# Kernel tuning notes

Hardware: AMD Instinct MI355X
Metric: run time of the kernel (lower is better)

Reference implementation:

```python
import jax, jax.numpy as jnp
import numpy as np

NUM_NODES = 100000
NUM_EDGES = 50000
NUM_CONN = 800000
IN_DIM = 256
HIDDEN = 128
EDGE_ATTR_DIM = 17
LN_EPS = 1e-5


def setup_inputs() -> dict:
    key = jax.random.key(0)
    k1, k2, k3, kw1, kb1, kg, kbeta, kw2, kb2 = jax.random.split(key, 9)
    node_features = jax.random.normal(k1, (NUM_NODES, IN_DIM), dtype=jnp.float32)
    nodes = jax.random.randint(k2, (NUM_CONN,), 0, NUM_NODES, dtype=jnp.int64)
    edges = jax.random.randint(k3, (NUM_CONN,), 0, NUM_EDGES, dtype=jnp.int64)
    hyperedge_index = jnp.stack([nodes, edges], axis=0)
    # MLP params (Linear(in,hid) -> LayerNorm -> ReLU -> Dropout(eval:identity) -> Linear(hid,out))
    W1 = jax.random.normal(kw1, (IN_DIM, HIDDEN), dtype=jnp.float32) * (1.0 / np.sqrt(IN_DIM))
    b1 = jax.random.normal(kb1, (HIDDEN,), dtype=jnp.float32) * 0.01
    ln_g = jnp.ones((HIDDEN,), dtype=jnp.float32)
    ln_b = jnp.zeros((HIDDEN,), dtype=jnp.float32)
    W2 = jax.random.normal(kw2, (HIDDEN, EDGE_ATTR_DIM), dtype=jnp.float32) * (1.0 / np.sqrt(HIDDEN))
    b2 = jax.random.normal(kb2, (EDGE_ATTR_DIM,), dtype=jnp.float32) * 0.01
    return {"node_features": node_features, "hyperedge_index": hyperedge_index,
            "W1": W1, "b1": b1, "ln_g": ln_g, "ln_b": ln_b, "W2": W2, "b2": b2}


def reference(node_features, hyperedge_index, W1, b1, ln_g, ln_b, W2, b2):
    nodes = hyperedge_index[0]
    edges = hyperedge_index[1]
    # indices are in-range by construction (torch valid_mask is all-True here)
    gathered = node_features[nodes]                         # [num_conn, in_dim]
    summed = jax.ops.segment_sum(gathered, edges, num_segments=NUM_EDGES)
    counts = jax.ops.segment_sum(jnp.ones(edges.shape, node_features.dtype), edges,
                                 num_segments=NUM_EDGES)
    edge_features = summed / jnp.clip(counts, 1.0)[:, None]  # mean aggregation
    # decoder MLP (dropout inactive in eval)
    h = edge_features @ W1 + b1
    mu = jnp.mean(h, axis=-1, keepdims=True)
    var = jnp.mean(jnp.square(h - mu), axis=-1, keepdims=True)
    h = (h - mu) * jax.lax.rsqrt(var + LN_EPS) * ln_g + ln_b
    h = jax.nn.relu(h)
    return h @ W2 + b2                                      # [num_edges, edge_attr_dim]
```

## Files before the change

kernel.cpp:

```cpp
#include <hip/hip_runtime.h>
#include <hip/hip_bf16.h>
#include <stdint.h>

#define NUM_NODES 100000
#define NUM_EDGES 50000
#define NUM_CONN  800000
#define IN_DIM    256
#define HIDDEN    128
#define EDGE_DIM  17
#define PAD       64

typedef __bf16 bf16x8 __attribute__((ext_vector_type(8)));
typedef float  f32x4  __attribute__((ext_vector_type(4)));


__global__ void prep_kernel(const float* __restrict__ W1, const float* __restrict__ W2,
                            __bf16* __restrict__ w1f, __bf16* __restrict__ w2f,
                            int* __restrict__ counts) {
    int i = blockIdx.x * 256 + threadIdx.x;
    if (i < NUM_EDGES) counts[i] = 0;
    if (i < 4096) {
        int lane = i & 63, t = (i >> 6) & 7, kc2 = i >> 9;
        int m = lane & 15, q = lane >> 4;
        int n = t * 16 + m;
        int kbase = kc2 * 32 + q * 8;
        __bf16* dst = w1f + (size_t)i * 8;
        #pragma unroll
        for (int ki = 0; ki < 8; ++ki)
            dst[ki] = (__bf16)W1[(size_t)(kbase + ki) * HIDDEN + n];
    } else if (i < 4608) {
        int f = i - 4096;
        int lane = f & 63, t = (f >> 6) & 1, ks = f >> 7;
        int m = lane & 15, q = lane >> 4;
        int n = t * 16 + m;
        int kbase = ks * 32 + q * 8;
        __bf16* dst = w2f + (size_t)f * 8;
        #pragma unroll
        for (int ki = 0; ki < 8; ++ki)
            dst[ki] = (n < EDGE_DIM) ? (__bf16)W2[(size_t)(kbase + ki) * EDGE_DIM + n]
                                     : (__bf16)0.0f;
    }
}

#define FRONT_BLOCKS 1173
__global__ __launch_bounds__(256) void front_kernel(const int* __restrict__ idx,
        int stride, int* __restrict__ counts, int* __restrict__ slots,
        const float* __restrict__ nf, const __bf16* __restrict__ w1f,
        __bf16* __restrict__ pbf) {
    __shared__ __align__(16) __bf16 lds_w[32768];
    const int d3 = blockIdx.x / 3, r3 = blockIdx.x % 3;
    if (r3 == 1) {
        long c0 = ((long)d3 * 256 + threadIdx.x) * 8;
        if (c0 < NUM_CONN) {
            int nd[8], ed[8];
            if (stride == 2) {
                #pragma unroll
                for (int k = 0; k < 4; ++k) {
                    int4 vn = ((const int4*)idx)[c0 / 2 + k];
                    int4 ve = ((const int4*)(idx + 2 * NUM_CONN))[c0 / 2 + k];
                    nd[2 * k] = vn.x; nd[2 * k + 1] = vn.z;
                    ed[2 * k] = ve.x; ed[2 * k + 1] = ve.z;
                }
            } else {
                #pragma unroll
                for (int k = 0; k < 8; ++k) {
                    nd[k] = idx[c0 + k];
                    ed[k] = idx[NUM_CONN + c0 + k];
                }
            }
            int pos[8];
            #pragma unroll
            for (int k = 0; k < 8; ++k) pos[k] = atomicAdd(&counts[ed[k]], 1);
            #pragma unroll
            for (int k = 0; k < 8; ++k)
                if (pos[k] < PAD) slots[(size_t)ed[k] * PAD + pos[k]] = nd[k];
        }
        return;
    }
    const int p = 2 * d3 + (r3 == 2 ? 1 : 0);
    {
        const uint4* src = (const uint4*)w1f;
        uint4* dst = (uint4*)lds_w;
        #pragma unroll
        for (int i = threadIdx.x; i < 4096; i += 256) dst[i] = src[i];
    }
    __syncthreads();

    const int wave = threadIdx.x >> 6;
    const int lane = threadIdx.x & 63;
    const int m = lane & 15, q = lane >> 4;
    const int rowbase = p * 128 + wave * 32;
    const bf16x8* frag = (const bf16x8*)lds_w;

    const float* ap[2];
    #pragma unroll
    for (int mt = 0; mt < 2; ++mt) {
        int r = rowbase + mt * 16 + m;
        if (r >= NUM_NODES) r = NUM_NODES - 1;
        ap[mt] = nf + (size_t)r * IN_DIM + q * 8;
    }

    f32x4 acc[2][8];
    #pragma unroll
    for (int mt = 0; mt < 2; ++mt)
        #pragma unroll
        for (int t = 0; t < 8; ++t) acc[mt][t] = (f32x4){0.f, 0.f, 0.f, 0.f};

    float4 a4[16];
    #pragma unroll
    for (int kc2 = 0; kc2 < 8; ++kc2) {
        a4[2 * kc2]     = *(const float4*)(ap[0] + kc2 * 32);
        a4[2 * kc2 + 1] = *(const float4*)(ap[0] + kc2 * 32 + 4);
    }

    #pragma unroll
    for (int mt = 0; mt < 2; ++mt) {
        bf16x8 afr[8];
        #pragma unroll
        for (int kc2 = 0; kc2 < 8; ++kc2) {
            float4 f0 = a4[2 * kc2], f1 = a4[2 * kc2 + 1];
            afr[kc2][0] = (__bf16)f0.x; afr[kc2][1] = (__bf16)f0.y;
            afr[kc2][2] = (__bf16)f0.z; afr[kc2][3] = (__bf16)f0.w;
            afr[kc2][4] = (__bf16)f1.x; afr[kc2][5] = (__bf16)f1.y;
            afr[kc2][6] = (__bf16)f1.z; afr[kc2][7] = (__bf16)f1.w;
        }
        if (mt == 0) {
            #pragma unroll
            for (int kc2 = 0; kc2 < 8; ++kc2) {
                a4[2 * kc2]     = *(const float4*)(ap[1] + kc2 * 32);
                a4[2 * kc2 + 1] = *(const float4*)(ap[1] + kc2 * 32 + 4);
            }
        }
        #pragma unroll
        for (int kc2 = 0; kc2 < 8; ++kc2) {
            #pragma unroll
            for (int t = 0; t < 8; ++t)
                acc[mt][t] = __builtin_amdgcn_mfma_f32_16x16x32_bf16(
                    afr[kc2], frag[(kc2 * 8 + t) * 64 + lane], acc[mt][t], 0, 0, 0);
        }
    }

    #pragma unroll
    for (int mt = 0; mt < 2; ++mt) {
        int ob = rowbase + mt * 16 + q * 4;
        #pragma unroll
        for (int t = 0; t < 8; ++t)
            #pragma unroll
            for (int r = 0; r < 4; ++r) {
                int orow = ob + r;
                if (orow < NUM_NODES)
                    pbf[(size_t)orow * HIDDEN + t * 16 + m] = (__bf16)acc[mt][t][r];
            }
    }
}

__global__ __launch_bounds__(256) void edge_kernel(const uint4* __restrict__ p4,
        const int* __restrict__ counts, const int* __restrict__ slots,
        const float* __restrict__ b1, const float* __restrict__ ln_g,
        const float* __restrict__ ln_b, const __bf16* __restrict__ w2f,
        const float* __restrict__ b2, float* __restrict__ out) {
    __shared__ __align__(16) uint4 lds_r[256];
    const int wave = threadIdx.x >> 6;
    const int lane = threadIdx.x & 63;
    const int g = lane & 15, ge = lane >> 4;
    const int el = wave * 4 + ge;
    const int e = blockIdx.x * 16 + el;

    const int c = counts[e];
    const int cc = c < PAD ? c : PAD;
    const float inv = 1.0f / (float)(c > 0 ? c : 1);

    float acc[8];
    #pragma unroll
    for (int d = 0; d < 8; ++d) acc[d] = 0.f;

    for (int c0 = 0; c0 < cc; c0 += 16) {
        int slv = slots[(size_t)e * PAD + c0 + g];
        int lim = cc - c0; if (lim > 16) lim = 16;
        if (lim == 16) {
            #pragma unroll
            for (int k0 = 0; k0 < 16; k0 += 4) {
                uint4 u[4];
                #pragma unroll
                for (int k = 0; k < 4; ++k) {
                    int nd = __shfl(slv, ge * 16 + k0 + k, 64);
                    u[k] = p4[(size_t)nd * 16 + g];
                }
                #pragma unroll
                for (int k = 0; k < 4; ++k) {
                    acc[0] += __uint_as_float(u[k].x << 16);
                    acc[1] += __uint_as_float(u[k].x & 0xffff0000u);
                    acc[2] += __uint_as_float(u[k].y << 16);
                    acc[3] += __uint_as_float(u[k].y & 0xffff0000u);
                    acc[4] += __uint_as_float(u[k].z << 16);
                    acc[5] += __uint_as_float(u[k].z & 0xffff0000u);
                    acc[6] += __uint_as_float(u[k].w << 16);
                    acc[7] += __uint_as_float(u[k].w & 0xffff0000u);
                }
            }
        } else {
            for (int k0 = 0; k0 < lim; k0 += 4) {
                uint4 u[4];
                unsigned okm[4];
                #pragma unroll
                for (int k = 0; k < 4; ++k) {
                    int nd = __shfl(slv, ge * 16 + k0 + k, 64);
                    nd = ((unsigned)nd < NUM_NODES) ? nd : 0;
                    u[k] = p4[(size_t)nd * 16 + g];
                    okm[k] = (k0 + k < lim) ? 0xffffffffu : 0u;
                }
                #pragma unroll
                for (int k = 0; k < 4; ++k) {
                    uint4 v = u[k];
                    v.x &= okm[k]; v.y &= okm[k]; v.z &= okm[k]; v.w &= okm[k];
                    acc[0] += __uint_as_float(v.x << 16);
                    acc[1] += __uint_as_float(v.x & 0xffff0000u);
                    acc[2] += __uint_as_float(v.y << 16);
                    acc[3] += __uint_as_float(v.y & 0xffff0000u);
                    acc[4] += __uint_as_float(v.z << 16);
                    acc[5] += __uint_as_float(v.z & 0xffff0000u);
                    acc[6] += __uint_as_float(v.w << 16);
                    acc[7] += __uint_as_float(v.w & 0xffff0000u);
                }
            }
        }
    }

    float4 bA = ((const float4*)b1)[2 * g];
    float4 bB = ((const float4*)b1)[2 * g + 1];
    float h[8];
    h[0] = acc[0] * inv + bA.x; h[1] = acc[1] * inv + bA.y;
    h[2] = acc[2] * inv + bA.z; h[3] = acc[3] * inv + bA.w;
    h[4] = acc[4] * inv + bB.x; h[5] = acc[5] * inv + bB.y;
    h[6] = acc[6] * inv + bB.z; h[7] = acc[7] * inv + bB.w;

    float s = 0.f;
    #pragma unroll
    for (int d = 0; d < 8; ++d) s += h[d];
    #pragma unroll
    for (int off = 8; off > 0; off >>= 1) s += __shfl_xor(s, off, 64);
    float mu = s * (1.0f / 128.0f);

    float dv[8], vv = 0.f;
    #pragma unroll
    for (int d = 0; d < 8; ++d) { dv[d] = h[d] - mu; vv += dv[d] * dv[d]; }
    #pragma unroll
    for (int off = 8; off > 0; off >>= 1) vv += __shfl_xor(vv, off, 64);
    float rs = rsqrtf(vv * (1.0f / 128.0f) + 1e-5f);

    float4 gA = ((const float4*)ln_g)[2 * g];
    float4 gB = ((const float4*)ln_g)[2 * g + 1];
    float4 eA = ((const float4*)ln_b)[2 * g];
    float4 eB = ((const float4*)ln_b)[2 * g + 1];
    float gg[8] = {gA.x, gA.y, gA.z, gA.w, gB.x, gB.y, gB.z, gB.w};
    float ee[8] = {eA.x, eA.y, eA.z, eA.w, eB.x, eB.y, eB.z, eB.w};
    union { __bf16 b[8]; uint4 u; } pk;
    #pragma unroll
    for (int d = 0; d < 8; ++d) {
        float r = dv[d] * rs * gg[d] + ee[d];
        pk.b[d] = (__bf16)(r > 0.f ? r : 0.f);
    }
    lds_r[el * 16 + g] = pk.u;
    __syncthreads();

    if (wave == 0) {
        const int m = lane & 15, q = lane >> 4;
        const __bf16* lr = (const __bf16*)lds_r;
        const bf16x8* fw = (const bf16x8*)w2f;
        f32x4 a0 = (f32x4){0.f, 0.f, 0.f, 0.f};
        f32x4 a1 = (f32x4){0.f, 0.f, 0.f, 0.f};
        #pragma unroll
        for (int ks = 0; ks < 4; ++ks) {
            bf16x8 a = *(const bf16x8*)(lr + m * 128 + ks * 32 + q * 8);
            a0 = __builtin_amdgcn_mfma_f32_16x16x32_bf16(a, fw[(ks * 2 + 0) * 64 + lane], a0, 0, 0, 0);
            a1 = __builtin_amdgcn_mfma_f32_16x16x32_bf16(a, fw[(ks * 2 + 1) * 64 + lane], a1, 0, 0, 0);
        }
        int rowb = blockIdx.x * 16 + q * 4;
        float bm = b2[m];
        float b16 = b2[16];
        #pragma unroll
        for (int r = 0; r < 4; ++r) {
            out[(size_t)(rowb + r) * EDGE_DIM + m] = a0[r] + bm;
            if (m == 0) out[(size_t)(rowb + r) * EDGE_DIM + 16] = a1[r] + b16;
        }
    }
}

extern "C" void kernel_launch(void* const* d_in, const int* in_sizes, int n_in,
                              void* d_out, int out_size, void* d_ws, size_t ws_size,
                              hipStream_t stream) {
    const float* nf  = (const float*)d_in[0];
    const int*   idx = (const int*)d_in[1];
    const float* W1  = (const float*)d_in[2];
    const float* b1  = (const float*)d_in[3];
    const float* g   = (const float*)d_in[4];
    const float* be  = (const float*)d_in[5];
    const float* W2  = (const float*)d_in[6];
    const float* b2  = (const float*)d_in[7];
    float* out = (float*)d_out;

    char* ws = (char*)d_ws;
    __bf16* P      = (__bf16*)ws;
    int*    counts = (int*)(ws + 25600000);
    int*    slots  = (int*)(ws + 25800000);
    __bf16* W1F    = (__bf16*)(ws + 38600000);
    __bf16* W2F    = (__bf16*)(ws + 38665536);

    int stride = (in_sizes[1] == 2 * NUM_CONN) ? 1 : 2;

    prep_kernel<<<196, 256, 0, stream>>>(W1, W2, W1F, W2F, counts);
    front_kernel<<<FRONT_BLOCKS, 256, 0, stream>>>(idx, stride, counts, slots, nf, W1F, P);
    edge_kernel<<<NUM_EDGES / 16, 256, 0, stream>>>((const uint4*)P, counts, slots,
                                                    b1, g, be, W2F, b2, out);
}
```

Measured before the change: 257.8 us.

## Halve front kernel tile and LDS weight buffer, stream W1 in two phases

The fused front kernel now gives each GEMM block 64 node rows instead of 128 and holds only half of the W1 fragments in LDS at a time, reloading the second half after the first output pass. The block count and the interleave of scatter blocks change to match (4 GEMM blocks per scatter block), and launch bounds ask for 4 blocks per CU. The W1 copy into LDS now overlaps the loading of node features. The goal is higher occupancy and less LDS and register pressure. The cost is W1 being loaded twice per block, extra barriers, and more blocks overall.

Measured after the change: 238.5 us. -7.5%, faster.

```diff
diff --git a/kernel.cpp b/kernel.cpp
--- a/kernel.cpp
+++ b/kernel.cpp
@@ -42,15 +42,15 @@
     }
 }
 
-#define FRONT_BLOCKS 1173
-__global__ __launch_bounds__(256) void front_kernel(const int* __restrict__ idx,
+#define FRONT_BLOCKS 1955
+__global__ __launch_bounds__(256, 4) void front_kernel(const int* __restrict__ idx,
         int stride, int* __restrict__ counts, int* __restrict__ slots,
         const float* __restrict__ nf, const __bf16* __restrict__ w1f,
         __bf16* __restrict__ pbf) {
-    __shared__ __align__(16) __bf16 lds_w[32768];
-    const int d3 = blockIdx.x / 3, r3 = blockIdx.x % 3;
-    if (r3 == 1) {
-        long c0 = ((long)d3 * 256 + threadIdx.x) * 8;
+    __shared__ __align__(16) __bf16 lds_w[16384];
+    const int nb = blockIdx.x / 5, r5 = blockIdx.x % 5;
+    if (r5 == 2) {
+        long c0 = ((long)nb * 256 + threadIdx.x) * 8;
         if (c0 < NUM_CONN) {
             int nd[8], ed[8];
             if (stride == 2) {
@@ -77,80 +77,87 @@
         }
         return;
     }
-    const int p = 2 * d3 + (r3 == 2 ? 1 : 0);
-    {
-        const uint4* src = (const uint4*)w1f;
-        uint4* dst = (uint4*)lds_w;
-        #pragma unroll
-        for (int i = threadIdx.x; i < 4096; i += 256) dst[i] = src[i];
-    }
-    __syncthreads();
-
+    const int p = blockIdx.x - nb - (r5 > 2 ? 1 : 0);
     const int wave = threadIdx.x >> 6;
     const int lane = threadIdx.x & 63;
     const int m = lane & 15, q = lane >> 4;
-    const int rowbase = p * 128 + wave * 32;
-    const bf16x8* frag = (const bf16x8*)lds_w;
-
-    const float* ap[2];
-    #pragma unroll
-    for (int mt = 0; mt < 2; ++mt) {
-        int r = rowbase + mt * 16 + m;
-        if (r >= NUM_NODES) r = NUM_NODES - 1;
-        ap[mt] = nf + (size_t)r * IN_DIM + q * 8;
-    }
-
-    f32x4 acc[2][8];
-    #pragma unroll
-    for (int mt = 0; mt < 2; ++mt)
-        #pragma unroll
-        for (int t = 0; t < 8; ++t) acc[mt][t] = (f32x4){0.f, 0.f, 0.f, 0.f};
-
-    float4 a4[16];
-    #pragma unroll
-    for (int kc2 = 0; kc2 < 8; ++kc2) {
-        a4[2 * kc2]     = *(const float4*)(ap[0] + kc2 * 32);
-        a4[2 * kc2 + 1] = *(const float4*)(ap[0] + kc2 * 32 + 4);
-    }
-
-    #pragma unroll
-    for (int mt = 0; mt < 2; ++mt) {
-        bf16x8 afr[8];
-        #pragma unroll
-        for (int kc2 = 0; kc2 < 8; ++kc2) {
+    int row = p * 64 + wave * 16 + m;
+    if (row >= NUM_NODES) row = NUM_NODES - 1;
+    const float* ap = nf + (size_t)row * IN_DIM + q * 8;
+
+    const uint4* src = (const uint4*)w1f;
+    uint4* dst = (uint4*)lds_w;
+
+    bf16x8 afr[8];
+    {
+        float4 a4[8];
+        #pragma unroll
+        for (int kc2 = 0; kc2 < 4; ++kc2) {
+            a4[2 * kc2]     = *(const float4*)(ap + kc2 * 32);
+            a4[2 * kc2 + 1] = *(const float4*)(ap + kc2 * 32 + 4);
+        }
+        #pragma unroll
+        for (int i = threadIdx.x; i < 2048; i += 256) {
+            int kc2 = i >> 8, tt = (i >> 6) & 3, l = i & 63;
+            dst[i] = src[(kc2 * 8 + tt) * 64 + l];
+        }
+        #pragma unroll
+        for (int kc2 = 0; kc2 < 4; ++kc2) {
             float4 f0 = a4[2 * kc2], f1 = a4[2 * kc2 + 1];
             afr[kc2][0] = (__bf16)f0.x; afr[kc2][1] = (__bf16)f0.y;
             afr[kc2][2] = (__bf16)f0.z; afr[kc2][3] = (__bf16)f0.w;
             afr[kc2][4] = (__bf16)f1.x; afr[kc2][5] = (__bf16)f1.y;
             afr[kc2][6] = (__bf16)f1.z; afr[kc2][7] = (__bf16)f1.w;
         }
-        if (mt == 0) {
-            #pragma unroll
-            for (int kc2 = 0; kc2 < 8; ++kc2) {
-                a4[2 * kc2]     = *(const float4*)(ap[1] + kc2 * 32);
-                a4[2 * kc2 + 1] = *(const float4*)(ap[1] + kc2 * 32 + 4);
-            }
-        }
+        #pragma unroll
+        for (int kc2 = 4; kc2 < 8; ++kc2) {
+            a4[2 * (kc2 - 4)]     = *(const float4*)(ap + kc2 * 32);
+            a4[2 * (kc2 - 4) + 1] = *(const float4*)(ap + kc2 * 32 + 4);
+        }
+        #pragma unroll
+        for (int kc2 = 4; kc2 < 8; ++kc2) {
+            float4 f0 = a4[2 * (kc2 - 4)], f1 = a4[2 * (kc2 - 4) + 1];
+            afr[kc2][0] = (__bf16)f0.x; afr[kc2][1] = (__bf16)f0.y;
+            afr[kc2][2] = (__bf16)f0.z; afr[kc2][3] = (__bf16)f0.w;
+            afr[kc2][4] = (__bf16)f1.x; afr[kc2][5] = (__bf16)f1.y;
+            afr[kc2][6] = (__bf16)f1.z; afr[kc2][7] = (__bf16)f1.w;
+        }
+    }
+    __syncthreads();
+
+    const bf16x8* frag = (const bf16x8*)lds_w;
+    #pragma unroll
+    for (int ph = 0; ph < 2; ++ph) {
+        f32x4 acc[4];
+        #pragma unroll
+        for (int tt = 0; tt < 4; ++tt) acc[tt] = (f32x4){0.f, 0.f, 0.f, 0.f};
         #pragma unroll
         for (int kc2 = 0; kc2 < 8; ++kc2) {
             #pragma unroll
-            for (int t = 0; t < 8; ++t)
-                acc[mt][t] = __builtin_amdgcn_mfma_f32_16x16x32_bf16(
-                    afr[kc2], frag[(kc2 * 8 + t) * 64 + lane], acc[mt][t], 0, 0, 0);
-        }
-    }
-
-    #pragma unroll
-    for (int mt = 0; mt < 2; ++mt) {
-        int ob = rowbase + mt * 16 + q * 4;
-        #pragma unroll
-        for (int t = 0; t < 8; ++t)
+            for (int tt = 0; tt < 4; ++tt)
+                acc[tt] = __builtin_amdgcn_mfma_f32_16x16x32_bf16(
+                    afr[kc2], frag[(kc2 * 4 + tt) * 64 + lane], acc[tt], 0, 0, 0);
+        }
+        int ob = p * 64 + wave * 16 + q * 4;
+        #pragma unroll
+        for (int tt = 0; tt < 4; ++tt) {
+            int col = (ph * 4 + tt) * 16 + m;
             #pragma unroll
             for (int r = 0; r < 4; ++r) {
                 int orow = ob + r;
                 if (orow < NUM_NODES)
-                    pbf[(size_t)orow * HIDDEN + t * 16 + m] = (__bf16)acc[mt][t][r];
-            }
+                    pbf[(size_t)orow * HIDDEN + col] = (__bf16)acc[tt][r];
+            }
+        }
+        if (ph == 0) {
+            __syncthreads();
+            #pragma unroll
+            for (int i = threadIdx.x; i < 2048; i += 256) {
+                int kc2 = i >> 8, tt = (i >> 6) & 3, l = i & 63;
+                dst[i] = src[(kc2 * 8 + 4 + tt) * 64 + l];
+            }
+            __syncthreads();
+        }
     }
 }
 
```
